# Kernel tuning notes

Hardware: AMD Instinct MI355X
Metric: run time of the kernel (lower is better)

The kernel has to match this reference:

```python
import jax, jax.numpy as jnp
import numpy as np

TAU = 0.01          # gumbel_softmax temperature
EPS = 1e-7          # tf.keras.backend.epsilon()
DEPTH = 5
N_NODES = 2 ** DEPTH - 1   # 31 internal nodes
N_LEAVES = 2 ** DEPTH      # 32 leaves


def _build_route():
    # route[l, node + dir*N_NODES] = 1 along the root-to-leaf path of leaf l
    # (same structure old_route_to_new_route produces for a perfect tree)
    route = np.zeros((N_LEAVES, 2 * N_NODES), dtype=np.float32)
    for l in range(N_LEAVES):
        node = 0
        for d in range(DEPTH):
            bit = (l >> (DEPTH - 1 - d)) & 1  # 0 = left, 1 = right
            route[l, node + bit * N_NODES] = 1.0
            node = 2 * node + 1 + bit
    return route


def setup_inputs() -> dict:
    B, F, T = 32768, 128, 100
    key = jax.random.key(0)
    k1, k2, k3, k4 = jax.random.split(key, 4)
    x = jax.random.normal(k1, (B, F), dtype=jnp.float32)
    kernel = jax.random.normal(k2, (T, F, N_NODES), dtype=jnp.float32) * 0.1
    bias = jax.random.normal(k3, (T, N_NODES), dtype=jnp.float32) * 0.1
    leaf = jax.random.normal(k4, (T, N_LEAVES), dtype=jnp.float32)
    route = jnp.asarray(_build_route())  # [L, 2N], shared tree topology
    return {"x": x, "kernel": kernel, "bias": bias, "leaf": leaf, "route": route}


def reference(x, kernel, bias, leaf, route):
    # NodeLayer: matmul(x, concat([K, -K], 1)) + concat([b, -b], 0)
    h = jnp.einsum("bf,tfn->btn", x, kernel) + bias          # [B, T, N]
    h2 = jnp.concatenate([h, -h], axis=-1)                   # [B, T, 2N]
    # activation1: log(clip(sigmoid(clip(h/tau, -32, 32)), eps, 1))
    a1 = jnp.log(jnp.clip(jax.nn.sigmoid(jnp.clip(h2 / TAU, -32.0, 32.0)), EPS, 1.0))
    # route aggregation: sum log-probs along each root->leaf path
    r = jnp.einsum("btm,lm->btl", a1, route)                 # [B, T, L]
    # activation2: exp(clip(., -32, 0)) -> leaf routing probabilities
    probs = jnp.exp(jnp.clip(r, -32.0, 0.0))
    # weight leaf values by route probabilities, sum over leaves and trees
    return jnp.einsum("btl,tl->b", probs, leaf)              # [B] raw GBM output
```

## Files before the change

### kernel.cpp

```cpp
#include <hip/hip_runtime.h>

typedef _Float16 f16x8  __attribute__((ext_vector_type(8)));
typedef float    f32x16 __attribute__((ext_vector_type(16)));
typedef float    f32x4  __attribute__((ext_vector_type(4)));

#define NTREES  100
#define WAVES   8
#define TPG     50
#define NCH     7
#define BM      64
#define KS      9
#define TSTRIDE (KS * 512)
#define NSCALE  (-144.269504088896f)

__device__ __forceinline__ int node_of_row(int sr, float& sg) {
  const int h   = (sr >> 2) & 1;
  const int reg = (sr & 3) + ((sr >> 3) << 2);
  sg = 1.0f;
  if (reg == 0) { if (h) sg = -1.0f; return 0; }
  if (reg == 1) return 1 + h;
  if (reg < 4)  return 1 + 2 * h + reg;
  if (reg < 8)  return 3 + 4 * h + reg;
  return 7 + 8 * h + reg;
}

__device__ __forceinline__ float exp2_fast(float v) {
#if __has_builtin(__builtin_amdgcn_exp2f)
  return __builtin_amdgcn_exp2f(v);
#else
  return exp2f(v);
#endif
}

__device__ __forceinline__ float sigl(float zn) {
  float e = exp2_fast(zn);
  return __builtin_amdgcn_rcpf(1.0f + e);
}

__global__ void prep_b(const float* __restrict__ kern, const float* __restrict__ bias,
                       unsigned short* __restrict__ bws) {
  __shared__ float kt[128][32];
  __shared__ float bs[32];
  const int t = blockIdx.x, tid = threadIdx.x;
  const float* src = kern + (size_t)t * (128 * 31);
  for (int i = tid; i < 128 * 32; i += 512) {
    const int f = i >> 5, sr_ = i & 31;
    float sg; const int g = node_of_row(sr_, sg);
    kt[f][sr_] = src[f * 31 + g] * (NSCALE * sg);
  }
  if (tid < 32) {
    float sg; const int g = node_of_row(tid, sg);
    bs[tid] = bias[t * 31 + g] * (NSCALE * sg);
  }
  __syncthreads();
  unsigned short* dst = bws + (size_t)t * TSTRIDE;
  for (int s = tid; s < KS * 64; s += 512) {
    const int ks = s >> 6, lane = s & 63;
    const int row = lane & 31;
    const int k0 = ks * 16 + ((lane >> 5) << 3);
    f16x8 o;
    if (ks < 8) {
      #pragma unroll
      for (int j = 0; j < 8; ++j) o[j] = (_Float16)kt[k0 + j][row];
    } else {
      #pragma unroll
      for (int j = 0; j < 8; ++j) o[j] = (_Float16)0.0f;
      if (lane < 32) o[0] = (_Float16)bs[row];
    }
    *(f16x8*)(dst + s * 8) = o;
  }
}

__device__ __forceinline__ float half_eval(const f32x16& a, const f32x4& L0,
                                           const f32x4& L1, const f32x4& L2,
                                           const f32x4& L3) {
  float sl, sr;
  const float c0 = sigl(a[0]);
  sl = sigl(a[1]); sr = 1.0f - sl;
  const float a0 = c0 * sl, a1 = c0 * sr;
  sl = sigl(a[2]); sr = 1.0f - sl;
  const float b0 = a0 * sl, b1 = a0 * sr;
  sl = sigl(a[3]); sr = 1.0f - sl;
  const float b2 = a1 * sl, b3 = a1 * sr;
  float cum[8];
  sl = sigl(a[4]); sr = 1.0f - sl; cum[0] = b0 * sl; cum[1] = b0 * sr;
  sl = sigl(a[5]); sr = 1.0f - sl; cum[2] = b1 * sl; cum[3] = b1 * sr;
  sl = sigl(a[6]); sr = 1.0f - sl; cum[4] = b2 * sl; cum[5] = b2 * sr;
  sl = sigl(a[7]); sr = 1.0f - sl; cum[6] = b3 * sl; cum[7] = b3 * sr;
  float s = 0.0f;
  s = fmaf(cum[0], fmaf(sigl(a[8]),  L0[0] - L0[1], L0[1]), s);
  s = fmaf(cum[1], fmaf(sigl(a[9]),  L0[2] - L0[3], L0[3]), s);
  s = fmaf(cum[2], fmaf(sigl(a[10]), L1[0] - L1[1], L1[1]), s);
  s = fmaf(cum[3], fmaf(sigl(a[11]), L1[2] - L1[3], L1[3]), s);
  s = fmaf(cum[4], fmaf(sigl(a[12]), L2[0] - L2[1], L2[1]), s);
  s = fmaf(cum[5], fmaf(sigl(a[13]), L2[2] - L2[3], L2[3]), s);
  s = fmaf(cum[6], fmaf(sigl(a[14]), L3[0] - L3[1], L3[1]), s);
  s = fmaf(cum[7], fmaf(sigl(a[15]), L3[2] - L3[3], L3[3]), s);
  return s;
}

__global__ __launch_bounds__(512, 4) void gbm_main(
    const float* __restrict__ x,
    const unsigned short* __restrict__ bws,
    const float* __restrict__ leaf,
    float* __restrict__ out)
{
  __shared__ __align__(16) unsigned char lds[2 * KS * 64 * 16];
  float* red = (float*)lds;

  const int tid  = threadIdx.x;
  const int lane = tid & 63;
  const int w    = tid >> 6;
  const int g    = blockIdx.y;
  const int rowbase = blockIdx.x * BM;

  #pragma unroll
  for (int T = 0; T < 2; ++T)
    for (int s = tid; s < KS * 64; s += 512) {
      const int ks = s >> 6, l = s & 63;
      f16x8 h8;
      if (ks < 8) {
        const int xrow = (l & 31) + T * 32;
        const int k0 = ks * 16 + ((l >> 5) << 3);
        const float* px = x + (size_t)(rowbase + xrow) * 128 + k0;
        float4 v0 = *(const float4*)px;
        float4 v1 = *(const float4*)(px + 4);
        h8[0] = (_Float16)v0.x; h8[1] = (_Float16)v0.y;
        h8[2] = (_Float16)v0.z; h8[3] = (_Float16)v0.w;
        h8[4] = (_Float16)v1.x; h8[5] = (_Float16)v1.y;
        h8[6] = (_Float16)v1.z; h8[7] = (_Float16)v1.w;
      } else {
        #pragma unroll
        for (int j = 0; j < 8; ++j) h8[j] = (_Float16)0.0f;
        if (l < 32) h8[0] = (_Float16)1.0f;
      }
      *(f16x8*)(lds + T * (KS * 64 * 16) + s * 16) = h8;
    }

  f16x8 br[KS];
  {
    const unsigned short* bt = bws + (size_t)(g * TPG + w) * TSTRIDE;
    #pragma unroll
    for (int i = 0; i < KS; ++i)
      br[i] = *(const f16x8*)(bt + (size_t)i * 512 + lane * 8);
  }

  __syncthreads();

  const int h = lane >> 5;
  float outAcc0 = 0.0f, outAcc1 = 0.0f;

  for (int c = 0; c < NCH; ++c) {
    const int ti  = c * WAVES + w;
    const bool act = ti < TPG;

    if (act) {
      const int tree = g * TPG + ti;
      const float* lp = leaf + (size_t)tree * 32 + (h << 4);
      f32x4 L0 = *(const f32x4*)lp;
      f32x4 L1 = *(const f32x4*)(lp + 4);
      f32x4 L2 = *(const f32x4*)(lp + 8);
      f32x4 L3 = *(const f32x4*)(lp + 12);

      f32x16 a0 = {};
      __builtin_amdgcn_s_setprio(1);
      #pragma unroll
      for (int ks = 0; ks < KS; ++ks) {
        f16x8 bx = *(const f16x8*)(lds + (ks * 64 + lane) * 16);
        a0 = __builtin_amdgcn_mfma_f32_32x32x16_f16(br[ks], bx, a0, 0, 0, 0);
      }
      __builtin_amdgcn_s_setprio(0);
      outAcc0 += half_eval(a0, L0, L1, L2, L3);

      f32x16 a1 = {};
      __builtin_amdgcn_s_setprio(1);
      #pragma unroll
      for (int ks = 0; ks < KS; ++ks) {
        f16x8 bx = *(const f16x8*)(lds + KS * 64 * 16 + (ks * 64 + lane) * 16);
        a1 = __builtin_amdgcn_mfma_f32_32x32x16_f16(br[ks], bx, a1, 0, 0, 0);
      }
      __builtin_amdgcn_s_setprio(0);

      if ((c + 1) * WAVES + w < TPG) {
        const unsigned short* nb =
            bws + (size_t)(g * TPG + (c + 1) * WAVES + w) * TSTRIDE;
        #pragma unroll
        for (int i = 0; i < KS; ++i)
          br[i] = *(const f16x8*)(nb + (size_t)i * 512 + lane * 8);
      }

      outAcc1 += half_eval(a1, L0, L1, L2, L3);
    } else if ((c + 1) * WAVES + w < TPG) {
      const unsigned short* nb =
          bws + (size_t)(g * TPG + (c + 1) * WAVES + w) * TSTRIDE;
      #pragma unroll
      for (int i = 0; i < KS; ++i)
        br[i] = *(const f16x8*)(nb + (size_t)i * 512 + lane * 8);
    }
  }

  __syncthreads();
  red[tid] = outAcc0;
  red[512 + tid] = outAcc1;
  __syncthreads();
  if (tid < BM) {
    const int tile = tid >> 5, r = tid & 31;
    float s = 0.0f;
    #pragma unroll
    for (int j = 0; j < 16; ++j)
      s += red[tile * 512 + j * 32 + r];
    atomicAdd(out + rowbase + tid, s);
  }
}

extern "C" void kernel_launch(void* const* d_in, const int* in_sizes, int n_in,
                              void* d_out, int out_size, void* d_ws, size_t ws_size,
                              hipStream_t stream) {
  const float* x    = (const float*)d_in[0];
  const float* kern = (const float*)d_in[1];
  const float* bias = (const float*)d_in[2];
  const float* leaf = (const float*)d_in[3];

  unsigned short* bws = (unsigned short*)d_ws;

  prep_b<<<NTREES, 512, 0, stream>>>(kern, bias, bws);
  hipMemsetAsync(d_out, 0, (size_t)out_size * sizeof(float), stream);
  gbm_main<<<dim3(32768 / BM, 2), 512, 0, stream>>>(x, bws, leaf, (float*)d_out);
}
```

Baseline: 53.52 us.

## Software-pipeline MFMA tiles with sigmoid evaluation and remove divergent tree branches

Restructures the per-chunk loop so the MFMA for the next tile (next tree's first half, current tree's second half) is issued before the sigmoid/leaf evaluation of the previous accumulator. This lets the matrix core overlap with the VALU transcendental work. Inactive trees are now clamped to a valid index and masked with a 0/1 multiplier instead of branching. The cost is redundant work for the padded trees in the last chunk and higher register pressure from keeping two accumulators live. The s_setprio hints are dropped.

```diff
diff --git a/kernel.cpp b/kernel.cpp
--- a/kernel.cpp
+++ b/kernel.cpp
@@ -99,6 +99,17 @@
   return s;
 }
 
+__device__ __forceinline__ f32x16 mfma_tile(const unsigned char* lds, int toff,
+                                            int lane, const f16x8* br) {
+  f32x16 a = {};
+  #pragma unroll
+  for (int ks = 0; ks < KS; ++ks) {
+    f16x8 bx = *(const f16x8*)(lds + toff + (ks * 64 + lane) * 16);
+    a = __builtin_amdgcn_mfma_f32_32x32x16_f16(br[ks], bx, a, 0, 0, 0);
+  }
+  return a;
+}
+
 __global__ __launch_bounds__(512, 4) void gbm_main(
     const float* __restrict__ x,
     const unsigned short* __restrict__ bws,
@@ -150,53 +161,37 @@
   const int h = lane >> 5;
   float outAcc0 = 0.0f, outAcc1 = 0.0f;
 
+  f32x16 aP = mfma_tile(lds, 0, lane, br);
+  f32x16 aQ;
+
   for (int c = 0; c < NCH; ++c) {
-    const int ti  = c * WAVES + w;
-    const bool act = ti < TPG;
-
-    if (act) {
-      const int tree = g * TPG + ti;
-      const float* lp = leaf + (size_t)tree * 32 + (h << 4);
-      f32x4 L0 = *(const f32x4*)lp;
-      f32x4 L1 = *(const f32x4*)(lp + 4);
-      f32x4 L2 = *(const f32x4*)(lp + 8);
-      f32x4 L3 = *(const f32x4*)(lp + 12);
-
-      f32x16 a0 = {};
-      __builtin_amdgcn_s_setprio(1);
-      #pragma unroll
-      for (int ks = 0; ks < KS; ++ks) {
-        f16x8 bx = *(const f16x8*)(lds + (ks * 64 + lane) * 16);
-        a0 = __builtin_amdgcn_mfma_f32_32x32x16_f16(br[ks], bx, a0, 0, 0, 0);
-      }
-      __builtin_amdgcn_s_setprio(0);
-      outAcc0 += half_eval(a0, L0, L1, L2, L3);
-
-      f32x16 a1 = {};
-      __builtin_amdgcn_s_setprio(1);
-      #pragma unroll
-      for (int ks = 0; ks < KS; ++ks) {
-        f16x8 bx = *(const f16x8*)(lds + KS * 64 * 16 + (ks * 64 + lane) * 16);
-        a1 = __builtin_amdgcn_mfma_f32_32x32x16_f16(br[ks], bx, a1, 0, 0, 0);
-      }
-      __builtin_amdgcn_s_setprio(0);
-
-      if ((c + 1) * WAVES + w < TPG) {
-        const unsigned short* nb =
-            bws + (size_t)(g * TPG + (c + 1) * WAVES + w) * TSTRIDE;
-        #pragma unroll
-        for (int i = 0; i < KS; ++i)
-          br[i] = *(const f16x8*)(nb + (size_t)i * 512 + lane * 8);
-      }
-
-      outAcc1 += half_eval(a1, L0, L1, L2, L3);
-    } else if ((c + 1) * WAVES + w < TPG) {
+    const int ti   = c * WAVES + w;
+    const float actf = (ti < TPG) ? 1.0f : 0.0f;
+    const int tree = g * TPG + ((ti < TPG) ? ti : (TPG - 1));
+
+    const float* lp = leaf + (size_t)tree * 32 + (h << 4);
+    f32x4 L0 = *(const f32x4*)lp;
+    f32x4 L1 = *(const f32x4*)(lp + 4);
+    f32x4 L2 = *(const f32x4*)(lp + 8);
+    f32x4 L3 = *(const f32x4*)(lp + 12);
+
+    aQ = mfma_tile(lds, KS * 64 * 16, lane, br);
+
+    if (c + 1 < NCH) {
+      const int tin = (c + 1) * WAVES + w;
       const unsigned short* nb =
-          bws + (size_t)(g * TPG + (c + 1) * WAVES + w) * TSTRIDE;
+          bws + (size_t)(g * TPG + ((tin < TPG) ? tin : (TPG - 1))) * TSTRIDE;
       #pragma unroll
       for (int i = 0; i < KS; ++i)
         br[i] = *(const f16x8*)(nb + (size_t)i * 512 + lane * 8);
     }
+
+    outAcc0 += actf * half_eval(aP, L0, L1, L2, L3);
+
+    if (c + 1 < NCH)
+      aP = mfma_tile(lds, 0, lane, br);
+
+    outAcc1 += actf * half_eval(aQ, L0, L1, L2, L3);
   }
 
   __syncthreads();
```

Measured after the change: 78.48 us. 1.47x slower.
